# Kernel optimization log

Measured on AMD Instinct MI355X. Metric: run time of the kernel, lower is better.

The kernel has to match this reference:

```python
import jax, jax.numpy as jnp
import numpy as np

E = 1024
H = 16
HD = 64
LN_EPS = 1e-5


def _layernorm(x, g, b):
    mu = jnp.mean(x, axis=-1, keepdims=True)
    var = jnp.mean((x - mu) ** 2, axis=-1, keepdims=True)
    return (x - mu) * jax.lax.rsqrt(var + LN_EPS) * g + b


def _positional(L):
    # PositionalEncoding: stepper = 1/10000^(arange(0,E,2)/E); cat(sin, cos) -> [L, E]
    stepper = 1.0 / (10000.0 ** (jnp.arange(0, E, 2, dtype=jnp.float32) / E))
    args = jnp.arange(L, dtype=jnp.float32)[:, None] * stepper[None, :]  # [L, E/2]
    return jnp.concatenate([jnp.sin(args), jnp.cos(args)], axis=1)  # [L, E]


def setup_inputs() -> dict:
    key = jax.random.key(0)
    ks = jax.random.split(key, 8)
    s = 1.0 / np.sqrt(E)
    return {
        "sequences": jax.random.normal(ks[0], (4, 2048, E), dtype=jnp.float32),
        "W_q": jax.random.normal(ks[1], (E, E), dtype=jnp.float32) * s,
        "W_k": jax.random.normal(ks[2], (E, E), dtype=jnp.float32) * s,
        "W_v": jax.random.normal(ks[3], (E, E), dtype=jnp.float32) * s,
        "W_o": jax.random.normal(ks[4], (E, E), dtype=jnp.float32) * s,
        "ln1_g": jnp.ones((E,), jnp.float32),
        "ln1_b": jnp.zeros((E,), jnp.float32),
        "lin_W": jax.random.normal(ks[5], (E, E), dtype=jnp.float32) * s,  # torch Linear weight [out,in]
        "lin_b": jnp.zeros((E,), jnp.float32),
        "ln2_g": jnp.ones((E,), jnp.float32),
        "ln2_b": jnp.zeros((E,), jnp.float32),
    }


def reference(sequences, W_q, W_k, W_v, W_o, ln1_g, ln1_b, lin_W, lin_b, ln2_g, ln2_b):
    B, L, _ = sequences.shape
    x = sequences + _positional(L)[None]  # add positional embeddings
    # projections (no bias)
    q = (x @ W_q).reshape(B, L, H, HD).transpose(0, 2, 1, 3)  # [B,H,L,hd]
    k = (x @ W_k).reshape(B, L, H, HD).transpose(0, 2, 1, 3)
    v = (x @ W_v).reshape(B, L, H, HD).transpose(0, 2, 1, 3)
    # linear (softmax-free) attention: (Q K^T / sqrt(hd)) V
    scores = jnp.einsum("bhqd,bhkd->bhqk", q, k) / jnp.sqrt(jnp.float32(HD))
    ctx = jnp.einsum("bhqk,bhkd->bhqd", scores, v)
    ctx = ctx.transpose(0, 2, 1, 3).reshape(B, L, E)
    attn_out = ctx @ W_o
    h = _layernorm(x + attn_out, ln1_g, ln1_b)
    ff = jax.nn.relu(h @ lin_W.T + lin_b)
    return _layernorm(ff + h, ln2_g, ln2_b)
```

## Files before the change

### kernel.cpp

```cpp
#include <hip/hip_runtime.h>
#include <cstdint>

typedef unsigned short u16;
typedef __bf16 bf16x8 __attribute__((ext_vector_type(8)));
typedef float f32x4 __attribute__((ext_vector_type(4)));

__device__ __forceinline__ u16 f2bf(float f) {
    unsigned u = __float_as_uint(f);
    u += 0x7fffu + ((u >> 16) & 1u);
    return (u16)(u >> 16);
}
__device__ __forceinline__ float bf2f(u16 h) {
    return __uint_as_float(((unsigned)h) << 16);
}

__device__ __forceinline__ void lds16(const void* g, void* l) {
    __builtin_amdgcn_global_load_lds(
        (const __attribute__((address_space(1))) void*)g,
        (__attribute__((address_space(3))) void*)l, 16, 0, 0);
}

__device__ __forceinline__ float pos_term(int l, int e) {
    const float c = -13.287712379549449f / 512.0f;
    int ii = e & 511;
    float st  = exp2f(c * (float)ii);
    float arg = (float)l * st;
    return (e < 512) ? sinf(arg) : cosf(arg);
}

__global__ __launch_bounds__(256) void prep_all(const float* __restrict__ seq,
                                                const float* __restrict__ wq,
                                                const float* __restrict__ wk,
                                                const float* __restrict__ wv,
                                                const float* __restrict__ wl,
                                                u16* __restrict__ xb,
                                                u16* __restrict__ wt) {
    const int bx = blockIdx.x;
    if (bx < 8192) {
        size_t i = (size_t)bx * 256 + threadIdx.x;
        int e4 = (int)(i & 255) * 4;
        int l  = (int)((i >> 8) & 2047);
        float4 s = ((const float4*)seq)[i];
        float v[4] = {s.x, s.y, s.z, s.w};
#pragma unroll
        for (int j = 0; j < 4; j++) v[j] += pos_term(l, e4 + j);
        ushort4 ob; ob.x = f2bf(v[0]); ob.y = f2bf(v[1]); ob.z = f2bf(v[2]); ob.w = f2bf(v[3]);
        ((ushort4*)xb)[i] = ob;
        return;
    }
    const int idx = bx - 8192;
    const int mat = idx >> 10, bxw = idx & 1023;
    const int gx = bxw & 31, gy = bxw >> 5;
    const int tx = threadIdx.x & 31, ty = threadIdx.x >> 5;
    const float* src = (mat == 0) ? wq : (mat == 1) ? wk : (mat == 2) ? wv : wl;
    u16* dst = wt + (size_t)mat * 1024 * 1024;
    if (mat == 0 || mat == 3) {
        int col = gx * 32 + tx, row0 = gy * 32;
#pragma unroll
        for (int j = 0; j < 32; j += 8)
            dst[(size_t)(row0 + ty + j) * 1024 + col] = f2bf(src[(size_t)(row0 + ty + j) * 1024 + col]);
    } else {
        __shared__ float tile[32][33];
        int col = gx * 32 + tx, row0 = gy * 32;
#pragma unroll
        for (int j = 0; j < 32; j += 8)
            tile[ty + j][tx] = src[(size_t)(row0 + ty + j) * 1024 + col];
        __syncthreads();
        int col2 = gy * 32 + tx, row20 = gx * 32;
#pragma unroll
        for (int j = 0; j < 32; j += 8)
            dst[(size_t)(row20 + ty + j) * 1024 + col2] = f2bf(tile[tx][ty + j]);
    }
}

__global__ __launch_bounds__(256, 1) void gemm256q(const u16* __restrict__ A,
                                                   const u16* __restrict__ Bt,
                                                   u16* __restrict__ C,
                                                   int N, int K, int lda) {
    __shared__ __align__(16) u16 lds[65536];
    const int t = threadIdx.x;
    const int ntn = N >> 8;
    const int nwg = gridDim.x;
    int bid = (int)blockIdx.x;
    bid = (bid & 7) * (nwg >> 3) + (bid >> 3);
    const int tm = bid / ntn, tn = bid - tm * ntn;
    const size_t m0 = (size_t)tm << 8, n0 = (size_t)tn << 8;
    const int w = t >> 6, lane = t & 63;
    const int wr = w >> 1, wc = w & 1;

    const int r0 = t >> 3;
    const int ksrc = (t & 7) ^ (r0 & 7);
    const u16* sA = A + (m0 + r0) * (size_t)lda + ksrc * 8;
    const u16* sB = Bt + (n0 + r0) * (size_t)K + ksrc * 8;
    const size_t stA = (size_t)32 * lda, stB = (size_t)32 * K;

#define STAGEQ(bb, ko)                                                        \
    do {                                                                      \
        u16* d_ = lds + (bb) * 32768 + (w << 9);                              \
        _Pragma("unroll")                                                     \
        for (int k_ = 0; k_ < 8; k_++) {                                      \
            lds16(sA + (ko) + k_ * stA, d_ + k_ * 2048);                      \
            lds16(sB + (ko) + k_ * stB, d_ + 16384 + k_ * 2048);              \
        }                                                                     \
    } while (0)

    const int kx = lane & 7;
    const int ks0 = (((lane >> 4) ^ kx) << 3);
    const int ks1 = (((4 + (lane >> 4)) ^ kx) << 3);
    const int arow = (wr << 7) + (lane & 15);
    const int brow = (wc << 7) + (lane & 15);

    f32x4 acc[8][8];
#pragma unroll
    for (int i = 0; i < 8; i++)
#pragma unroll
        for (int j = 0; j < 8; j++)
#pragma unroll
            for (int r = 0; r < 4; r++) acc[i][j][r] = 0.0f;

    const int NT = K >> 6;
    STAGEQ(0, 0);

    for (int kt = 0; kt < NT; kt++) {
        const int b = kt & 1;
        const u16* Lb = lds + b * 32768;
        asm volatile("" ::: "memory");
        if (kt + 1 < NT) {
            STAGEQ(b ^ 1, (size_t)(kt + 1) << 6);
            asm volatile("s_waitcnt vmcnt(16)" ::: "memory");
        } else {
            asm volatile("s_waitcnt vmcnt(0)" ::: "memory");
        }
        __builtin_amdgcn_s_barrier();
        asm volatile("" ::: "memory");

#pragma unroll
        for (int kc = 0; kc < 2; kc++) {
            const int ksl = kc ? ks1 : ks0;
            bf16x8 bfr[8];
#pragma unroll
            for (int j = 0; j < 8; j++)
                bfr[j] = *reinterpret_cast<const bf16x8*>(Lb + 16384 + ((brow + j * 16) << 6) + ksl);
            __builtin_amdgcn_s_setprio(1);
#pragma unroll
            for (int i = 0; i < 8; i++) {
                const bf16x8 af = *reinterpret_cast<const bf16x8*>(Lb + ((arow + i * 16) << 6) + ksl);
#pragma unroll
                for (int j = 0; j < 8; j++)
                    acc[i][j] = __builtin_amdgcn_mfma_f32_16x16x32_bf16(af, bfr[j], acc[i][j], 0, 0, 0);
            }
            __builtin_amdgcn_s_setprio(0);
        }
        asm volatile("" ::: "memory");
        __builtin_amdgcn_s_barrier();
    }
#undef STAGEQ

    const int crow = (lane >> 4) << 2, ccol = lane & 15;
#pragma unroll
    for (int i = 0; i < 8; i++)
#pragma unroll
        for (int j = 0; j < 8; j++) {
            size_t row = m0 + (wr << 7) + (i << 4) + crow;
            size_t col = n0 + (wc << 7) + (j << 4) + ccol;
#pragma unroll
            for (int r = 0; r < 4; r++)
                C[(row + r) * (size_t)N + col] = f2bf(acc[i][j][r]);
        }
}

template <int EPI>
__global__ __launch_bounds__(512) void gemm8p(const u16* __restrict__ A,
                                              const u16* __restrict__ Bt,
                                              void* __restrict__ Cv,
                                              const float* __restrict__ bias,
                                              int N, int K, int lda, size_t bstride) {
    __shared__ __align__(16) u16 lds[49152];
    const int t = threadIdx.x;
    const int ntn = N >> 8;
    const int nwg = gridDim.x;
    int bid = (int)blockIdx.x;
    bid = (bid & 7) * (nwg >> 3) + (bid >> 3);
    const int tm = bid / ntn, tn = bid - tm * ntn;
    const size_t m0 = (size_t)tm << 7, n0 = (size_t)tn << 8;
    const int w = t >> 6, lane = t & 63;
    const int wr = w >> 2, wc = w & 3;
    const u16* Bt_e = Bt + (bstride ? (m0 >> 11) * bstride : 0);

    const int r0 = t >> 3;
    const int ksrc = (t & 7) ^ (r0 & 7);
    const u16* sA0 = A + (m0 + r0) * (size_t)lda + ksrc * 8;
    const u16* sA1 = sA0 + (size_t)64 * lda;
    const u16* sB0 = Bt_e + (n0 + r0) * (size_t)K + ksrc * 8;
    const u16* sB1 = sB0 + (size_t)64 * K;
    const u16* sB2 = sB0 + (size_t)128 * K;
    const u16* sB3 = sB0 + (size_t)192 * K;
    u16* dstW = lds + (w << 9);

    const int ao = ((wr << 6) | (lane & 15)) << 6;
    const int bo = 8192 + ((((wc << 6) | (lane & 15))) << 6);
    const int kx = lane & 7;
    const int ks0 = (((lane >> 4) ^ kx) << 3);
    const int ks1 = (((4 + (lane >> 4)) ^ kx) << 3);

    f32x4 acc[4][4];
#pragma unroll
    for (int i = 0; i < 4; i++)
#pragma unroll
        for (int j = 0; j < 4; j++)
#pragma unroll
            for (int r = 0; r < 4; r++) acc[i][j][r] = 0.0f;

    const int NT = K >> 6;
    lds16(sA0, dstW);          lds16(sA1, dstW + 4096);
    lds16(sB0, dstW + 8192);   lds16(sB1, dstW + 12288);
    lds16(sB2, dstW + 16384);  lds16(sB3, dstW + 20480);

    for (int kt = 0; kt < NT; kt++) {
        const int b = kt & 1;
        asm volatile("" ::: "memory");
        if (kt + 1 < NT) {
            const size_t ko = (size_t)(kt + 1) << 6;
            u16* d = dstW + (b ^ 1) * 24576;
            lds16(sA0 + ko, d);          lds16(sA1 + ko, d + 4096);
            lds16(sB0 + ko, d + 8192);   lds16(sB1 + ko, d + 12288);
            lds16(sB2 + ko, d + 16384);  lds16(sB3 + ko, d + 20480);
            asm volatile("s_waitcnt vmcnt(6)" ::: "memory");
        } else {
            asm volatile("s_waitcnt vmcnt(0)" ::: "memory");
        }
        __builtin_amdgcn_s_barrier();
        asm volatile("" ::: "memory");
        const u16* Lb = lds + b * 24576;
#pragma unroll
        for (int kc = 0; kc < 2; kc++) {
            const int ksl = kc ? ks1 : ks0;
            bf16x8 af[4], bfr[4];
#pragma unroll
            for (int i = 0; i < 4; i++)
                af[i] = *reinterpret_cast<const bf16x8*>(Lb + ao + i * 1024 + ksl);
#pragma unroll
            for (int j = 0; j < 4; j++)
                bfr[j] = *reinterpret_cast<const bf16x8*>(Lb + bo + j * 1024 + ksl);
            __builtin_amdgcn_s_setprio(1);
#pragma unroll
            for (int i = 0; i < 4; i++)
#pragma unroll
                for (int j = 0; j < 4; j++)
                    acc[i][j] = __builtin_amdgcn_mfma_f32_16x16x32_bf16(af[i], bfr[j], acc[i][j], 0, 0, 0);
            __builtin_amdgcn_s_setprio(0);
        }
        asm volatile("" ::: "memory");
        __builtin_amdgcn_s_barrier();
    }

    const int crow = (lane >> 4) << 2, ccol = lane & 15;
#pragma unroll
    for (int i = 0; i < 4; i++)
#pragma unroll
        for (int j = 0; j < 4; j++) {
            size_t row = m0 + (wr << 6) + (i << 4) + crow;
            size_t col = n0 + (wc << 6) + (j << 4) + ccol;
#pragma unroll
            for (int r = 0; r < 4; r++) {
                float v = acc[i][j][r];
                if (EPI == 3) { v += bias[col]; v = fmaxf(v, 0.0f); }
                ((u16*)Cv)[(row + r) * (size_t)N + col] = f2bf(v);
            }
        }
}

template <bool ADDI>
__global__ __launch_bounds__(256) void gemm128(const u16* __restrict__ A,
                                               const u16* __restrict__ Bt,
                                               u16* __restrict__ C,
                                               int N, int K, int lda) {
    __shared__ __align__(16) u16 lds[32768];
    const int t = threadIdx.x;
    const int ntn = N >> 7;
    const int nwg = gridDim.x;
    int bid = (int)blockIdx.x;
    bid = (bid & 7) * (nwg >> 3) + (bid >> 3);
    const int tm = bid / ntn, tn = bid - tm * ntn;
    const size_t m0 = (size_t)tm << 7, n0 = (size_t)tn << 7;
    const int w = t >> 6, lane = t & 63;
    const int wr = w >> 1, wc = w & 1;

    const int r0 = t >> 3;
    const int ksrc = (t & 7) ^ (r0 & 7);
    const u16* sA = A + (m0 + r0) * (size_t)lda + ksrc * 8;
    const u16* sB = Bt + (n0 + r0) * (size_t)K + ksrc * 8;
    const size_t stA = (size_t)32 * lda, stB = (size_t)32 * K;

    const int kx = lane & 7;
    const int ks0 = (((lane >> 4) ^ kx) << 3);
    const int ks1 = (((4 + (lane >> 4)) ^ kx) << 3);
    const int ao = ((wr << 6) | (lane & 15)) << 6;
    const int bo = 8192 + ((((wc << 6) | (lane & 15))) << 6);

    f32x4 acc[4][4];
#pragma unroll
    for (int i = 0; i < 4; i++)
#pragma unroll
        for (int j = 0; j < 4; j++)
#pragma unroll
            for (int r = 0; r < 4; r++) acc[i][j][r] = 0.0f;

#define STAGE128(bb, ko)                                                      \
    do {                                                                      \
        u16* dA_ = lds + (bb) * 16384 + (w << 9);                             \
        u16* dB_ = dA_ + 8192;                                                \
        _Pragma("unroll")                                                     \
        for (int j_ = 0; j_ < 4; j_++) {                                      \
            lds16(sA + (ko) + j_ * stA, dA_ + j_ * 2048);                     \
            lds16(sB + (ko) + j_ * stB, dB_ + j_ * 2048);                     \
        }                                                                     \
    } while (0)

    const int NT = K >> 6;
    STAGE128(0, 0);
    for (int kt = 0; kt < NT; kt++) {
        const int b = kt & 1;
        asm volatile("" ::: "memory");
        if (kt + 1 < NT) {
            STAGE128(b ^ 1, (size_t)(kt + 1) << 6);
            asm volatile("s_waitcnt vmcnt(8)" ::: "memory");
        } else {
            asm volatile("s_waitcnt vmcnt(0)" ::: "memory");
        }
        __builtin_amdgcn_s_barrier();
        asm volatile("" ::: "memory");
        const u16* Lb = lds + b * 16384;
#pragma unroll
        for (int kc = 0; kc < 2; kc++) {
            const int ksl = kc ? ks1 : ks0;
            bf16x8 af[4], bfr[4];
#pragma unroll
            for (int i = 0; i < 4; i++)
                af[i] = *reinterpret_cast<const bf16x8*>(Lb + ao + i * 1024 + ksl);
#pragma unroll
            for (int j = 0; j < 4; j++)
                bfr[j] = *reinterpret_cast<const bf16x8*>(Lb + bo + j * 1024 + ksl);
            __builtin_amdgcn_s_setprio(1);
#pragma unroll
            for (int i = 0; i < 4; i++)
#pragma unroll
                for (int j = 0; j < 4; j++)
                    acc[i][j] = __builtin_amdgcn_mfma_f32_16x16x32_bf16(af[i], bfr[j], acc[i][j], 0, 0, 0);
            __builtin_amdgcn_s_setprio(0);
        }
        asm volatile("" ::: "memory");
        __builtin_amdgcn_s_barrier();
    }
#undef STAGE128

    const int crow = (lane >> 4) << 2, ccol = lane & 15;
#pragma unroll
    for (int i = 0; i < 4; i++)
#pragma unroll
        for (int j = 0; j < 4; j++) {
            size_t row = m0 + (wr << 6) + (i << 4) + crow;
            size_t col = n0 + (wc << 6) + (j << 4) + ccol;
#pragma unroll
            for (int r = 0; r < 4; r++) {
                float v = acc[i][j][r];
                if (ADDI && col == ((row + r) & 1023)) v += 1.0f;
                C[(row + r) * (size_t)N + col] = f2bf(v);
            }
        }
}

__global__ __launch_bounds__(256) void ktv_kernel(const u16* __restrict__ kv,
                                                  float* __restrict__ part) {
    const int bh = blockIdx.x, split = blockIdx.y;
    const int b = bh >> 4, h = bh & 15;
    const u16* Kp = kv + (size_t)b * 2048 * 2048 + h * 64;
    const u16* Vp = Kp + 1024;
    __shared__ float ks[8][64], vs[8][64];
    float acc[16];
#pragma unroll
    for (int i = 0; i < 16; i++) acc[i] = 0.0f;
    const int t = threadIdx.x, r = t >> 4, c = t & 15;
    const int lr = t >> 5, lc = (t & 31) * 2;
    for (int l0 = split * 128; l0 < split * 128 + 128; l0 += 8) {
        unsigned kk = *(const unsigned*)(Kp + (size_t)(l0 + lr) * 2048 + lc);
        unsigned vv = *(const unsigned*)(Vp + (size_t)(l0 + lr) * 2048 + lc);
        ks[lr][lc] = bf2f((u16)kk); ks[lr][lc + 1] = bf2f((u16)(kk >> 16));
        vs[lr][lc] = bf2f((u16)vv); vs[lr][lc + 1] = bf2f((u16)(vv >> 16));
        __syncthreads();
#pragma unroll
        for (int i = 0; i < 8; i++) {
            float kvr[4], vw[4];
#pragma unroll
            for (int a = 0; a < 4; a++) { kvr[a] = ks[i][r + 16 * a]; vw[a] = vs[i][c + 16 * a]; }
#pragma unroll
            for (int a = 0; a < 4; a++)
#pragma unroll
                for (int q = 0; q < 4; q++) acc[a * 4 + q] += kvr[a] * vw[q];
        }
        __syncthreads();
    }
    float* o = part + ((size_t)split * 64 + bh) * 4096;
#pragma unroll
    for (int a = 0; a < 4; a++)
#pragma unroll
        for (int q = 0; q < 4; q++) o[(r + 16 * a) * 64 + (c + 16 * q)] = acc[a * 4 + q];
}

__global__ __launch_bounds__(256) void ktv_reduce(const float* __restrict__ part,
                                                  float* __restrict__ ktv) {
    int i = blockIdx.x * 256 + threadIdx.x;
    float s = 0.0f;
#pragma unroll
    for (int sp = 0; sp < 16; sp++) s += part[(size_t)sp * 262144 + i];
    ktv[i] = s;
}

__global__ __launch_bounds__(256) void wprime_kernel(const float* __restrict__ ktv,
                                                     const float* __restrict__ Wo,
                                                     u16* __restrict__ wp) {
    const int n = blockIdx.x * 256 + threadIdx.x;
    const int h = blockIdx.y, b = blockIdx.z;
    const float* kt = ktv + ((size_t)(b * 16 + h) << 12);
    float acc[64];
#pragma unroll
    for (int i = 0; i < 64; i++) acc[i] = 0.0f;
    for (int j = 0; j < 64; j++) {
        float w = Wo[(size_t)(h * 64 + j) * 1024 + n];
#pragma unroll
        for (int i = 0; i < 64; i++) acc[i] += kt[i * 64 + j] * w;
    }
    u16* o = wp + ((size_t)b << 20) + (size_t)n * 1024 + h * 64;
    u16 ob[64];
#pragma unroll
    for (int i = 0; i < 64; i++) ob[i] = f2bf(acc[i] * 0.125f);
#pragma unroll
    for (int i = 0; i < 8; i++)
        ((uint4*)o)[i] = ((const uint4*)ob)[i];
}

__global__ __launch_bounds__(256) void ln1_kernel(const u16* __restrict__ xr,
                                                  const float* __restrict__ g,
                                                  const float* __restrict__ be,
                                                  u16* __restrict__ outB) {
    __shared__ float sm[4];
    const int row = blockIdx.x, t = threadIdx.x;
    const ushort4 xv = ((const ushort4*)(xr + (size_t)row * 1024))[t];
    float x0 = bf2f(xv.x), x1 = bf2f(xv.y), x2 = bf2f(xv.z), x3 = bf2f(xv.w);
    float s = x0 + x1 + x2 + x3;
#pragma unroll
    for (int off = 32; off > 0; off >>= 1) s += __shfl_down(s, off);
    if ((t & 63) == 0) sm[t >> 6] = s;
    __syncthreads();
    const float mean = (sm[0] + sm[1] + sm[2] + sm[3]) * (1.0f / 1024.0f);
    __syncthreads();
    x0 -= mean; x1 -= mean; x2 -= mean; x3 -= mean;
    float s2 = x0 * x0 + x1 * x1 + x2 * x2 + x3 * x3;
#pragma unroll
    for (int off = 32; off > 0; off >>= 1) s2 += __shfl_down(s2, off);
    if ((t & 63) == 0) sm[t >> 6] = s2;
    __syncthreads();
    const float var = (sm[0] + sm[1] + sm[2] + sm[3]) * (1.0f / 1024.0f);
    const float rs = rsqrtf(var + 1e-5f);
    const float4 gv = ((const float4*)g)[t];
    const float4 bv = ((const float4*)be)[t];
    ushort4 ob;
    ob.x = f2bf(x0 * rs * gv.x + bv.x);
    ob.y = f2bf(x1 * rs * gv.y + bv.y);
    ob.z = f2bf(x2 * rs * gv.z + bv.z);
    ob.w = f2bf(x3 * rs * gv.w + bv.w);
    ((ushort4*)(outB + (size_t)row * 1024))[t] = ob;
}

__global__ __launch_bounds__(256) void ln2_kernel(const u16* __restrict__ ff,
                                                  const u16* __restrict__ h1,
                                                  const float* __restrict__ g,
                                                  const float* __restrict__ be,
                                                  float* __restrict__ outF) {
    __shared__ float sm[4];
    const int row = blockIdx.x, t = threadIdx.x;
    const ushort4 fv = ((const ushort4*)(ff + (size_t)row * 1024))[t];
    const ushort4 hv = ((const ushort4*)(h1 + (size_t)row * 1024))[t];
    float x0 = bf2f(fv.x) + bf2f(hv.x), x1 = bf2f(fv.y) + bf2f(hv.y);
    float x2 = bf2f(fv.z) + bf2f(hv.z), x3 = bf2f(fv.w) + bf2f(hv.w);
    float s = x0 + x1 + x2 + x3;
#pragma unroll
    for (int off = 32; off > 0; off >>= 1) s += __shfl_down(s, off);
    if ((t & 63) == 0) sm[t >> 6] = s;
    __syncthreads();
    const float mean = (sm[0] + sm[1] + sm[2] + sm[3]) * (1.0f / 1024.0f);
    __syncthreads();
    x0 -= mean; x1 -= mean; x2 -= mean; x3 -= mean;
    float s2 = x0 * x0 + x1 * x1 + x2 * x2 + x3 * x3;
#pragma unroll
    for (int off = 32; off > 0; off >>= 1) s2 += __shfl_down(s2, off);
    if ((t & 63) == 0) sm[t >> 6] = s2;
    __syncthreads();
    const float var = (sm[0] + sm[1] + sm[2] + sm[3]) * (1.0f / 1024.0f);
    const float rs = rsqrtf(var + 1e-5f);
    const float4 gv = ((const float4*)g)[t];
    const float4 bv = ((const float4*)be)[t];
    float4 o;
    o.x = x0 * rs * gv.x + bv.x;
    o.y = x1 * rs * gv.y + bv.y;
    o.z = x2 * rs * gv.z + bv.z;
    o.w = x3 * rs * gv.w + bv.w;
    ((float4*)(outF + (size_t)row * 1024))[t] = o;
}

extern "C" void kernel_launch(void* const* d_in, const int* in_sizes, int n_in,
                              void* d_out, int out_size, void* d_ws, size_t ws_size,
                              hipStream_t stream) {
    const float* seq = (const float*)d_in[0];
    const float* Wq  = (const float*)d_in[1];
    const float* Wk  = (const float*)d_in[2];
    const float* Wv  = (const float*)d_in[3];
    const float* Wo  = (const float*)d_in[4];
    const float* g1  = (const float*)d_in[5];
    const float* b1  = (const float*)d_in[6];
    const float* Wl  = (const float*)d_in[7];
    const float* bl  = (const float*)d_in[8];
    const float* g2  = (const float*)d_in[9];
    const float* b2  = (const float*)d_in[10];

    char* ws = (char*)d_ws;
    const size_t MB = 1024 * 1024;
    u16*   x_bf    = (u16*)(ws + 0);
    u16*   wt      = (u16*)(ws + 16 * MB);
    u16*   kv      = (u16*)(ws + 24 * MB);
    float* kpart   = (float*)(ws + 56 * MB);
    u16*   attnres = (u16*)(ws + 56 * MB);
    float* ktv     = (float*)(ws + 72 * MB);
    u16*   wpr     = (u16*)(ws + 73 * MB);
    u16*   wcomb   = (u16*)(ws + 81 * MB);
    u16*   h1b     = (u16*)(ws + 89 * MB);
    u16*   ffb     = (u16*)(ws + 105 * MB);

    prep_all<<<dim3(8192 + 4096), dim3(256), 0, stream>>>(seq, Wq, Wk, Wv, Wl, x_bf, wt);
    gemm256q<<<dim3(256), dim3(256), 0, stream>>>(x_bf, wt + (size_t)1 * MB, kv,
                                                  2048, 1024, 1024);
    ktv_kernel<<<dim3(64, 16), dim3(256), 0, stream>>>(kv, kpart);
    ktv_reduce<<<dim3(1024), dim3(256), 0, stream>>>(kpart, ktv);
    wprime_kernel<<<dim3(4, 16, 4), dim3(256), 0, stream>>>(ktv, Wo, wpr);
    gemm128<true><<<dim3(256), dim3(256), 0, stream>>>(wpr, wt, wcomb, 1024, 1024, 1024);
    gemm8p<2><<<dim3(256), dim3(512), 0, stream>>>(x_bf, wcomb, attnres, nullptr,
                                                   1024, 1024, 1024, (size_t)1024 * 1024);
    ln1_kernel<<<dim3(8192), dim3(256), 0, stream>>>(attnres, g1, b1, h1b);
    gemm8p<3><<<dim3(256), dim3(512), 0, stream>>>(h1b, wt + (size_t)3 * MB, ffb,
                                                   bl, 1024, 1024, 1024, 0);
    ln2_kernel<<<dim3(8192), dim3(256), 0, stream>>>(ffb, h1b, g2, b2, (float*)d_out);
}
```

Before: 196.2 us.

## Compute K^T V via per-batch Gram matrix instead of materializing K and V

Rewrites K^T V = Wk^T (X^T X) Wv. The prep kernel now also writes a transposed bf16 copy of X, a Gram kernel computes X^T X per batch (1024x1024), a 1024^3 GEMM multiplies the Gram matrix by Wv, and a small kernel contracts with Wk per head. This replaces the large 8192x2048x1024 K/V projection GEMM plus the split reduction over sequence length with smaller per-batch 1024-sized GEMMs. It adds an extra transposed write of X and rounds the Gram matrix to bf16, which may change accuracy.

```diff
diff --git a/kernel.cpp b/kernel.cpp
--- a/kernel.cpp
+++ b/kernel.cpp
@@ -34,24 +34,44 @@
                                                 const float* __restrict__ wv,
                                                 const float* __restrict__ wl,
                                                 u16* __restrict__ xb,
+                                                u16* __restrict__ xt,
                                                 u16* __restrict__ wt) {
     const int bx = blockIdx.x;
-    if (bx < 8192) {
-        size_t i = (size_t)bx * 256 + threadIdx.x;
-        int e4 = (int)(i & 255) * 4;
-        int l  = (int)((i >> 8) & 2047);
-        float4 s = ((const float4*)seq)[i];
-        float v[4] = {s.x, s.y, s.z, s.w};
-#pragma unroll
-        for (int j = 0; j < 4; j++) v[j] += pos_term(l, e4 + j);
-        ushort4 ob; ob.x = f2bf(v[0]); ob.y = f2bf(v[1]); ob.z = f2bf(v[2]); ob.w = f2bf(v[3]);
-        ((ushort4*)xb)[i] = ob;
+    const int t = threadIdx.x;
+    if (bx < 4096) {
+        __shared__ u16 tb[64][33];
+        const int rt = bx >> 5, ct = bx & 31;
+        const int r0 = rt * 64, c0 = ct * 32;
+        const int r_l = t >> 2, c8 = (t & 3) * 8;
+        const int row = r0 + r_l, l = row & 2047;
+        const float* sp = seq + (size_t)row * 1024 + c0 + c8;
+        float4 a0 = ((const float4*)sp)[0];
+        float4 a1 = ((const float4*)sp)[1];
+        float v[8] = {a0.x, a0.y, a0.z, a0.w, a1.x, a1.y, a1.z, a1.w};
+        u16 ob[8];
+#pragma unroll
+        for (int jj = 0; jj < 8; jj++) {
+            v[jj] += pos_term(l, c0 + c8 + jj);
+            ob[jj] = f2bf(v[jj]);
+            tb[r_l][c8 + jj] = ob[jj];
+        }
+        u16* xp = xb + (size_t)row * 1024 + c0 + c8;
+        ((ushort4*)xp)[0] = *(const ushort4*)&ob[0];
+        ((ushort4*)xp)[1] = *(const ushort4*)&ob[4];
+        __syncthreads();
+        const int c_l = t >> 3, r8 = (t & 7) * 8;
+        u16 tv[8];
+#pragma unroll
+        for (int jj = 0; jj < 8; jj++) tv[jj] = tb[r8 + jj][c_l];
+        u16* tp = xt + (size_t)(c0 + c_l) * 8192 + r0 + r8;
+        ((ushort4*)tp)[0] = *(const ushort4*)&tv[0];
+        ((ushort4*)tp)[1] = *(const ushort4*)&tv[4];
         return;
     }
-    const int idx = bx - 8192;
+    const int idx = bx - 4096;
     const int mat = idx >> 10, bxw = idx & 1023;
     const int gx = bxw & 31, gy = bxw >> 5;
-    const int tx = threadIdx.x & 31, ty = threadIdx.x >> 5;
+    const int tx = t & 31, ty = t >> 5;
     const float* src = (mat == 0) ? wq : (mat == 1) ? wk : (mat == 2) ? wv : wl;
     u16* dst = wt + (size_t)mat * 1024 * 1024;
     if (mat == 0 || mat == 3) {
@@ -73,99 +93,100 @@
     }
 }
 
-__global__ __launch_bounds__(256, 1) void gemm256q(const u16* __restrict__ A,
-                                                   const u16* __restrict__ Bt,
-                                                   u16* __restrict__ C,
-                                                   int N, int K, int lda) {
-    __shared__ __align__(16) u16 lds[65536];
+__global__ __launch_bounds__(256) void gram_kernel(const u16* __restrict__ xt,
+                                                   u16* __restrict__ G) {
+    __shared__ __align__(16) u16 lds[32768];
     const int t = threadIdx.x;
-    const int ntn = N >> 8;
     const int nwg = gridDim.x;
     int bid = (int)blockIdx.x;
     bid = (bid & 7) * (nwg >> 3) + (bid >> 3);
-    const int tm = bid / ntn, tn = bid - tm * ntn;
-    const size_t m0 = (size_t)tm << 8, n0 = (size_t)tn << 8;
+    const int bt = bid >> 6, tile6 = bid & 63;
+    const int tm = tile6 >> 3, tn = tile6 & 7;
+    const size_t m0 = (size_t)tm << 7, n0 = (size_t)tn << 7;
     const int w = t >> 6, lane = t & 63;
     const int wr = w >> 1, wc = w & 1;
+    const size_t lda = 8192;
+    const u16* A = xt + (size_t)bt * 2048;
 
     const int r0 = t >> 3;
     const int ksrc = (t & 7) ^ (r0 & 7);
-    const u16* sA = A + (m0 + r0) * (size_t)lda + ksrc * 8;
-    const u16* sB = Bt + (n0 + r0) * (size_t)K + ksrc * 8;
-    const size_t stA = (size_t)32 * lda, stB = (size_t)32 * K;
-
-#define STAGEQ(bb, ko)                                                        \
-    do {                                                                      \
-        u16* d_ = lds + (bb) * 32768 + (w << 9);                              \
-        _Pragma("unroll")                                                     \
-        for (int k_ = 0; k_ < 8; k_++) {                                      \
-            lds16(sA + (ko) + k_ * stA, d_ + k_ * 2048);                      \
-            lds16(sB + (ko) + k_ * stB, d_ + 16384 + k_ * 2048);              \
-        }                                                                     \
-    } while (0)
+    const u16* sA = A + (m0 + r0) * lda + ksrc * 8;
+    const u16* sB = A + (n0 + r0) * lda + ksrc * 8;
+    const size_t st = (size_t)32 * lda;
 
     const int kx = lane & 7;
     const int ks0 = (((lane >> 4) ^ kx) << 3);
     const int ks1 = (((4 + (lane >> 4)) ^ kx) << 3);
-    const int arow = (wr << 7) + (lane & 15);
-    const int brow = (wc << 7) + (lane & 15);
-
-    f32x4 acc[8][8];
-#pragma unroll
-    for (int i = 0; i < 8; i++)
-#pragma unroll
-        for (int j = 0; j < 8; j++)
+    const int ao = ((wr << 6) | (lane & 15)) << 6;
+    const int bo = 8192 + ((((wc << 6) | (lane & 15))) << 6);
+
+    f32x4 acc[4][4];
+#pragma unroll
+    for (int i = 0; i < 4; i++)
+#pragma unroll
+        for (int j = 0; j < 4; j++)
 #pragma unroll
             for (int r = 0; r < 4; r++) acc[i][j][r] = 0.0f;
 
-    const int NT = K >> 6;
-    STAGEQ(0, 0);
-
+#define STAGEG(bb, ko)                                                        \
+    do {                                                                      \
+        u16* dA_ = lds + (bb) * 16384 + (w << 9);                             \
+        u16* dB_ = dA_ + 8192;                                                \
+        _Pragma("unroll")                                                     \
+        for (int j_ = 0; j_ < 4; j_++) {                                      \
+            lds16(sA + (ko) + j_ * st, dA_ + j_ * 2048);                      \
+            lds16(sB + (ko) + j_ * st, dB_ + j_ * 2048);                      \
+        }                                                                     \
+    } while (0)
+
+    const int NT = 32;
+    STAGEG(0, 0);
     for (int kt = 0; kt < NT; kt++) {
         const int b = kt & 1;
-        const u16* Lb = lds + b * 32768;
         asm volatile("" ::: "memory");
         if (kt + 1 < NT) {
-            STAGEQ(b ^ 1, (size_t)(kt + 1) << 6);
-            asm volatile("s_waitcnt vmcnt(16)" ::: "memory");
+            STAGEG(b ^ 1, (size_t)(kt + 1) << 6);
+            asm volatile("s_waitcnt vmcnt(8)" ::: "memory");
         } else {
             asm volatile("s_waitcnt vmcnt(0)" ::: "memory");
         }
         __builtin_amdgcn_s_barrier();
         asm volatile("" ::: "memory");
-
+        const u16* Lb = lds + b * 16384;
 #pragma unroll
         for (int kc = 0; kc < 2; kc++) {
             const int ksl = kc ? ks1 : ks0;
-            bf16x8 bfr[8];
-#pragma unroll
-            for (int j = 0; j < 8; j++)
-                bfr[j] = *reinterpret_cast<const bf16x8*>(Lb + 16384 + ((brow + j * 16) << 6) + ksl);
+            bf16x8 af[4], bfr[4];
+#pragma unroll
+            for (int i = 0; i < 4; i++)
+                af[i] = *reinterpret_cast<const bf16x8*>(Lb + ao + i * 1024 + ksl);
+#pragma unroll
+            for (int j = 0; j < 4; j++)
+                bfr[j] = *reinterpret_cast<const bf16x8*>(Lb + bo + j * 1024 + ksl);
             __builtin_amdgcn_s_setprio(1);
 #pragma unroll
-            for (int i = 0; i < 8; i++) {
-                const bf16x8 af = *reinterpret_cast<const bf16x8*>(Lb + ((arow + i * 16) << 6) + ksl);
-#pragma unroll
-                for (int j = 0; j < 8; j++)
-                    acc[i][j] = __builtin_amdgcn_mfma_f32_16x16x32_bf16(af, bfr[j], acc[i][j], 0, 0, 0);
-            }
+            for (int i = 0; i < 4; i++)
+#pragma unroll
+                for (int j = 0; j < 4; j++)
+                    acc[i][j] = __builtin_amdgcn_mfma_f32_16x16x32_bf16(af[i], bfr[j], acc[i][j], 0, 0, 0);
             __builtin_amdgcn_s_setprio(0);
         }
         asm volatile("" ::: "memory");
         __builtin_amdgcn_s_barrier();
     }
-#undef STAGEQ
-
+#undef STAGEG
+
+    u16* C = G + ((size_t)bt << 20);
     const int crow = (lane >> 4) << 2, ccol = lane & 15;
 #pragma unroll
-    for (int i = 0; i < 8; i++)
-#pragma unroll
-        for (int j = 0; j < 8; j++) {
-            size_t row = m0 + (wr << 7) + (i << 4) + crow;
-            size_t col = n0 + (wc << 7) + (j << 4) + ccol;
+    for (int i = 0; i < 4; i++)
+#pragma unroll
+        for (int j = 0; j < 4; j++) {
+            size_t row = m0 + (wr << 6) + (i << 4) + crow;
+            size_t col = n0 + (wc << 6) + (j << 4) + ccol;
 #pragma unroll
             for (int r = 0; r < 4; r++)
-                C[(row + r) * (size_t)N + col] = f2bf(acc[i][j][r]);
+                C[(row + r) * 1024 + col] = f2bf(acc[i][j][r]);
         }
 }
 
@@ -370,50 +391,40 @@
         }
 }
 
-__global__ __launch_bounds__(256) void ktv_kernel(const u16* __restrict__ kv,
-                                                  float* __restrict__ part) {
-    const int bh = blockIdx.x, split = blockIdx.y;
+__global__ __launch_bounds__(256) void ktv_small(const u16* __restrict__ T,
+                                                 const u16* __restrict__ WkT,
+                                                 float* __restrict__ ktv) {
+    const int bh = blockIdx.x, ig = blockIdx.y;
     const int b = bh >> 4, h = bh & 15;
-    const u16* Kp = kv + (size_t)b * 2048 * 2048 + h * 64;
-    const u16* Vp = Kp + 1024;
-    __shared__ float ks[8][64], vs[8][64];
+    const int t = threadIdx.x;
+    const int j = t & 63;
+    const int dq = __builtin_amdgcn_readfirstlane(t >> 6);
+    const u16* Tb = T + ((size_t)b * 1024) * 1024 + h * 64;
+    const u16* Wk = WkT + (size_t)(h * 64 + ig * 16) * 1024;
     float acc[16];
 #pragma unroll
     for (int i = 0; i < 16; i++) acc[i] = 0.0f;
-    const int t = threadIdx.x, r = t >> 4, c = t & 15;
-    const int lr = t >> 5, lc = (t & 31) * 2;
-    for (int l0 = split * 128; l0 < split * 128 + 128; l0 += 8) {
-        unsigned kk = *(const unsigned*)(Kp + (size_t)(l0 + lr) * 2048 + lc);
-        unsigned vv = *(const unsigned*)(Vp + (size_t)(l0 + lr) * 2048 + lc);
-        ks[lr][lc] = bf2f((u16)kk); ks[lr][lc + 1] = bf2f((u16)(kk >> 16));
-        vs[lr][lc] = bf2f((u16)vv); vs[lr][lc + 1] = bf2f((u16)(vv >> 16));
-        __syncthreads();
-#pragma unroll
-        for (int i = 0; i < 8; i++) {
-            float kvr[4], vw[4];
-#pragma unroll
-            for (int a = 0; a < 4; a++) { kvr[a] = ks[i][r + 16 * a]; vw[a] = vs[i][c + 16 * a]; }
-#pragma unroll
-            for (int a = 0; a < 4; a++)
-#pragma unroll
-                for (int q = 0; q < 4; q++) acc[a * 4 + q] += kvr[a] * vw[q];
-        }
-        __syncthreads();
-    }
-    float* o = part + ((size_t)split * 64 + bh) * 4096;
-#pragma unroll
-    for (int a = 0; a < 4; a++)
-#pragma unroll
-        for (int q = 0; q < 4; q++) o[(r + 16 * a) * 64 + (c + 16 * q)] = acc[a * 4 + q];
-}
-
-__global__ __launch_bounds__(256) void ktv_reduce(const float* __restrict__ part,
-                                                  float* __restrict__ ktv) {
-    int i = blockIdx.x * 256 + threadIdx.x;
-    float s = 0.0f;
-#pragma unroll
-    for (int sp = 0; sp < 16; sp++) s += part[(size_t)sp * 262144 + i];
-    ktv[i] = s;
+    const int d0 = dq * 256;
+    for (int d = d0; d < d0 + 256; d += 2) {
+        float tv0 = bf2f(Tb[(size_t)d * 1024 + j]);
+        float tv1 = bf2f(Tb[(size_t)(d + 1) * 1024 + j]);
+#pragma unroll
+        for (int i = 0; i < 16; i++) {
+            unsigned wv = *(const unsigned*)(Wk + i * 1024 + d);
+            acc[i] += bf2f((u16)wv) * tv0 + bf2f((u16)(wv >> 16)) * tv1;
+        }
+    }
+    __shared__ float red[4][16][64];
+#pragma unroll
+    for (int i = 0; i < 16; i++) red[t >> 6][i][j] = acc[i];
+    __syncthreads();
+    if (t < 64) {
+#pragma unroll
+        for (int i = 0; i < 16; i++) {
+            float s = red[0][i][j] + red[1][i][j] + red[2][i][j] + red[3][i][j];
+            ktv[((size_t)bh << 12) + (ig * 16 + i) * 64 + j] = s;
+        }
+    }
 }
 
 __global__ __launch_bounds__(256) void wprime_kernel(const float* __restrict__ ktv,
@@ -527,20 +538,22 @@
     const size_t MB = 1024 * 1024;
     u16*   x_bf    = (u16*)(ws + 0);
     u16*   wt      = (u16*)(ws + 16 * MB);
-    u16*   kv      = (u16*)(ws + 24 * MB);
-    float* kpart   = (float*)(ws + 56 * MB);
-    u16*   attnres = (u16*)(ws + 56 * MB);
-    float* ktv     = (float*)(ws + 72 * MB);
-    u16*   wpr     = (u16*)(ws + 73 * MB);
-    u16*   wcomb   = (u16*)(ws + 81 * MB);
+    u16*   xT      = (u16*)(ws + 24 * MB);
+    u16*   G       = (u16*)(ws + 40 * MB);
+    u16*   Tm      = (u16*)(ws + 48 * MB);
+    float* ktv     = (float*)(ws + 56 * MB);
+    u16*   wpr     = (u16*)(ws + 57 * MB);
+    u16*   wcomb   = (u16*)(ws + 65 * MB);
+    u16*   attnres = (u16*)(ws + 73 * MB);
     u16*   h1b     = (u16*)(ws + 89 * MB);
     u16*   ffb     = (u16*)(ws + 105 * MB);
 
-    prep_all<<<dim3(8192 + 4096), dim3(256), 0, stream>>>(seq, Wq, Wk, Wv, Wl, x_bf, wt);
-    gemm256q<<<dim3(256), dim3(256), 0, stream>>>(x_bf, wt + (size_t)1 * MB, kv,
-                                                  2048, 1024, 1024);
-    ktv_kernel<<<dim3(64, 16), dim3(256), 0, stream>>>(kv, kpart);
-    ktv_reduce<<<dim3(1024), dim3(256), 0, stream>>>(kpart, ktv);
+    prep_all<<<dim3(4096 + 4096), dim3(256), 0, stream>>>(seq, Wq, Wk, Wv, Wl,
+                                                          x_bf, xT, wt);
+    gram_kernel<<<dim3(256), dim3(256), 0, stream>>>(xT, G);
+    gemm128<false><<<dim3(256), dim3(256), 0, stream>>>(G, wt + (size_t)2 * MB, Tm,
+                                                        1024, 1024, 1024);
+    ktv_small<<<dim3(64, 4), dim3(256), 0, stream>>>(Tm, wt + (size_t)1 * MB, ktv);
     wprime_kernel<<<dim3(4, 16, 4), dim3(256), 0, stream>>>(ktv, Wo, wpr);
     gemm128<true><<<dim3(256), dim3(256), 0, stream>>>(wpr, wt, wcomb, 1024, 1024, 1024);
     gemm8p<2><<<dim3(256), dim3(512), 0, stream>>>(x_bf, wcomb, attnres, nullptr,
```

Measured after the change: 225.3 us. 14.8% more time.
